# Performance work log

Hardware: AMD Instinct MI355X
Metric: run time of the kernel (lower is better)

Reference implementation:

```python
import jax, jax.numpy as jnp
import numpy as np
from jax.scipy.ndimage import map_coordinates


def _so3_exp(w):
    # Rodrigues formula, small-angle safe. w: [B,3] -> [B,3,3]
    th = jnp.linalg.norm(w, axis=-1)
    small = th < 1e-6
    ths = jnp.where(small, 1.0, th)
    A = jnp.where(small, 1.0 - th * th / 6.0, jnp.sin(ths) / ths)
    Bc = jnp.where(small, 0.5 - th * th / 24.0, (1.0 - jnp.cos(ths)) / (ths * ths))
    wx, wy, wz = w[..., 0], w[..., 1], w[..., 2]
    z = jnp.zeros_like(wx)
    K = jnp.stack([
        jnp.stack([z, -wz, wy], -1),
        jnp.stack([wz, z, -wx], -1),
        jnp.stack([-wy, wx, z], -1),
    ], -2)
    I = jnp.eye(3, dtype=w.dtype)
    return I + A[..., None, None] * K + Bc[..., None, None] * (K @ K)


def _pose(rot, xyz, rt_inv, isocenter):
    # pivot about isocenter expressed in camera frame (transform_point(rt_inv^-1, iso))
    iso_h = jnp.concatenate([isocenter, jnp.ones((1,), isocenter.dtype)])
    c = (jnp.linalg.inv(rt_inv[0]) @ iso_h)[:3]
    I4 = jnp.eye(4, dtype=rot.dtype)
    pivot = I4.at[:3, 3].set(c)
    pivot_inv = I4.at[:3, 3].set(-c)
    R = _so3_exp(rot)[0]
    t = R @ xyz[0]  # einsum('bij,bj->bi', R, xyz)
    T = I4.at[:3, :3].set(R).at[:3, 3].set(t)
    return pivot @ T @ pivot_inv


def _render(volume, k_inv, ext, sdd, height, width, n_samples):
    # DRR: cast one ray per detector pixel from the source, trilinearly sample
    # the CT volume at n_samples midpoints along source->target, accumulate.
    Rw = ext[:3, :3]
    src = ext[:3, 3]
    u = jnp.arange(width, dtype=volume.dtype) + 0.5
    v = jnp.arange(height, dtype=volume.dtype) + 0.5
    uu, vv = jnp.meshgrid(u, v, indexing='xy')  # [H,W]
    pix = jnp.stack([uu, vv, jnp.ones_like(uu)], -1)  # [H,W,3]
    dirs = jnp.einsum('ij,hwj->hwi', k_inv[0], pix)  # camera-frame ray dirs
    tgt = src + sdd[0] * jnp.einsum('ij,hwj->hwi', Rw, dirs)  # detector points in world
    seg = tgt - src  # [H,W,3]
    tvals = (jnp.arange(n_samples, dtype=volume.dtype) + 0.5) / n_samples
    pts = src + tvals[:, None, None, None] * seg[None]  # [n,H,W,3] (voxel coords)
    step = jnp.linalg.norm(seg, axis=-1) / n_samples  # [H,W] per-sample path length
    vals = map_coordinates(volume, [pts[..., 0], pts[..., 1], pts[..., 2]],
                           order=1, mode='constant', cval=0.0)  # [n,H,W]
    img = vals.sum(0) * step
    return img[None, None]  # [1,1,H,W]


def setup_inputs() -> dict:
    key = jax.random.key(0)
    k1, k2, k3 = jax.random.split(key, 3)
    D = 256
    volume = jax.random.uniform(k1, (D, D, D), dtype=jnp.float32)
    isocenter = jnp.array([128.0, 128.0, 128.0], jnp.float32)
    sdd = jnp.array([600.0], jnp.float32)
    f, cx, cy = 850.0, 256.0, 256.0
    K = jnp.array([[f, 0.0, cx], [0.0, f, cy], [0.0, 0.0, 1.0]], jnp.float32)
    k_inv = jnp.linalg.inv(K)[None]
    rt_inv = jnp.eye(4, dtype=jnp.float32).at[:3, 3].set(
        jnp.array([128.0, 128.0, -472.0], jnp.float32))[None]
    rot = 1e-8 * jax.random.normal(k2, (1, 3), jnp.float32)
    xyz = 1e-8 * jax.random.normal(k3, (1, 3), jnp.float32)
    return {"volume": volume, "isocenter": isocenter, "rt_inv": rt_inv,
            "k_inv": k_inv, "sdd": sdd, "rot": rot, "xyz": xyz,
            "height": 512, "width": 512, "n_samples": 128}


def reference(volume, isocenter, rt_inv, k_inv, sdd, rot, xyz, height, width, n_samples):
    pose = _pose(rot, xyz, rt_inv, isocenter)
    ext = rt_inv[0] @ pose  # rt_inv @ pose
    return _render(volume, k_inv, ext, sdd, height, width, n_samples)
```

## Files before the change

### kernel.cpp

```cpp
#include <hip/hip_runtime.h>
#include <hip/hip_fp16.h>
#include <math.h>

#define VD 256
#define PAIR_BYTES (VD * VD * VD * 4UL)

__device__ inline __half2 u2h2(unsigned int p) {
    return *reinterpret_cast<__half2*>(&p);
}

__device__ inline void invert4x4(const float* m, float* inv) {
    inv[0]  =  m[5]*m[10]*m[15] - m[5]*m[11]*m[14] - m[9]*m[6]*m[15] + m[9]*m[7]*m[14] + m[13]*m[6]*m[11] - m[13]*m[7]*m[10];
    inv[4]  = -m[4]*m[10]*m[15] + m[4]*m[11]*m[14] + m[8]*m[6]*m[15] - m[8]*m[7]*m[14] - m[12]*m[6]*m[11] + m[12]*m[7]*m[10];
    inv[8]  =  m[4]*m[9]*m[15]  - m[4]*m[11]*m[13] - m[8]*m[5]*m[15] + m[8]*m[7]*m[13] + m[12]*m[5]*m[11] - m[12]*m[7]*m[9];
    inv[12] = -m[4]*m[9]*m[14]  + m[4]*m[10]*m[13] + m[8]*m[5]*m[14] - m[8]*m[6]*m[13] - m[12]*m[5]*m[10] + m[12]*m[6]*m[9];
    inv[1]  = -m[1]*m[10]*m[15] + m[1]*m[11]*m[14] + m[9]*m[2]*m[15] - m[9]*m[3]*m[14] - m[13]*m[2]*m[11] + m[13]*m[3]*m[10];
    inv[5]  =  m[0]*m[10]*m[15] - m[0]*m[11]*m[14] - m[8]*m[2]*m[15] + m[8]*m[3]*m[14] + m[12]*m[2]*m[11] - m[12]*m[3]*m[10];
    inv[9]  = -m[0]*m[9]*m[15]  + m[0]*m[11]*m[13] + m[8]*m[1]*m[15] - m[8]*m[3]*m[13] - m[12]*m[1]*m[11] + m[12]*m[3]*m[9];
    inv[13] =  m[0]*m[9]*m[14]  - m[0]*m[10]*m[13] - m[8]*m[1]*m[14] + m[8]*m[2]*m[13] + m[12]*m[1]*m[10] - m[12]*m[2]*m[9];
    inv[2]  =  m[1]*m[6]*m[15]  - m[1]*m[7]*m[14]  - m[5]*m[2]*m[15] + m[5]*m[3]*m[14] + m[13]*m[2]*m[7]  - m[13]*m[3]*m[6];
    inv[6]  = -m[0]*m[6]*m[15]  + m[0]*m[7]*m[14]  + m[4]*m[2]*m[15] - m[4]*m[3]*m[14] - m[12]*m[2]*m[7]  + m[12]*m[3]*m[6];
    inv[10] =  m[0]*m[5]*m[15]  - m[0]*m[7]*m[13]  - m[4]*m[1]*m[15] + m[4]*m[3]*m[13] + m[12]*m[1]*m[7]  - m[12]*m[3]*m[5];
    inv[14] = -m[0]*m[5]*m[14]  + m[0]*m[6]*m[13]  + m[4]*m[1]*m[14] - m[4]*m[2]*m[13] - m[12]*m[1]*m[6]  + m[12]*m[2]*m[5];
    inv[3]  = -m[1]*m[6]*m[11]  + m[1]*m[7]*m[10]  + m[5]*m[2]*m[11] - m[5]*m[3]*m[10] - m[9]*m[2]*m[7]   + m[9]*m[3]*m[6];
    inv[7]  =  m[0]*m[6]*m[11]  - m[0]*m[7]*m[10]  - m[4]*m[2]*m[11] + m[4]*m[3]*m[10] + m[8]*m[2]*m[7]   - m[8]*m[3]*m[6];
    inv[11] = -m[0]*m[5]*m[11]  + m[0]*m[7]*m[9]   + m[4]*m[1]*m[11] - m[4]*m[3]*m[9]  - m[8]*m[1]*m[7]   + m[8]*m[3]*m[5];
    inv[15] =  m[0]*m[5]*m[10]  - m[0]*m[6]*m[9]   - m[4]*m[1]*m[10] + m[4]*m[2]*m[9]  + m[8]*m[1]*m[6]   - m[8]*m[2]*m[5];
    float det = m[0]*inv[0] + m[1]*inv[4] + m[2]*inv[8] + m[3]*inv[12];
    float rdet = 1.0f / det;
    for (int i = 0; i < 16; i++) inv[i] *= rdet;
}

__device__ inline void compute_pose(const float* __restrict__ iso,
                                    const float* __restrict__ rt,
                                    const float* __restrict__ kinv,
                                    const float* __restrict__ sdd,
                                    const float* __restrict__ rot,
                                    const float* __restrict__ xyz,
                                    float* M, float* src3) {
    float m[16];
    for (int i = 0; i < 16; i++) m[i] = rt[i];
    float minv[16];
    invert4x4(m, minv);
    float c0 = minv[0]*iso[0] + minv[1]*iso[1] + minv[2]*iso[2]  + minv[3];
    float c1 = minv[4]*iso[0] + minv[5]*iso[1] + minv[6]*iso[2]  + minv[7];
    float c2 = minv[8]*iso[0] + minv[9]*iso[1] + minv[10]*iso[2] + minv[11];
    float wx = rot[0], wy = rot[1], wz = rot[2];
    float th2 = wx*wx + wy*wy + wz*wz;
    float th = sqrtf(th2);
    float Ac, Bc;
    if (th < 1e-6f) { Ac = 1.0f - th2 / 6.0f; Bc = 0.5f - th2 / 24.0f; }
    else            { Ac = sinf(th) / th;     Bc = (1.0f - cosf(th)) / th2; }
    float R[9];
    R[0] = 1.0f + Bc * (-(wy*wy + wz*wz));
    R[1] = Ac * (-wz) + Bc * (wx*wy);
    R[2] = Ac * ( wy) + Bc * (wx*wz);
    R[3] = Ac * ( wz) + Bc * (wx*wy);
    R[4] = 1.0f + Bc * (-(wx*wx + wz*wz));
    R[5] = Ac * (-wx) + Bc * (wy*wz);
    R[6] = Ac * (-wy) + Bc * (wx*wz);
    R[7] = Ac * ( wx) + Bc * (wy*wz);
    R[8] = 1.0f + Bc * (-(wx*wx + wy*wy));
    float tx = R[0]*xyz[0] + R[1]*xyz[1] + R[2]*xyz[2];
    float ty = R[3]*xyz[0] + R[4]*xyz[1] + R[5]*xyz[2];
    float tz = R[6]*xyz[0] + R[7]*xyz[1] + R[8]*xyz[2];
    float pt0 = c0 + tx - (R[0]*c0 + R[1]*c1 + R[2]*c2);
    float pt1 = c1 + ty - (R[3]*c0 + R[4]*c1 + R[5]*c2);
    float pt2 = c2 + tz - (R[6]*c0 + R[7]*c1 + R[8]*c2);
    float E[12];
    for (int i = 0; i < 3; i++) {
        for (int j = 0; j < 3; j++)
            E[i*4+j] = rt[i*4+0]*R[0*3+j] + rt[i*4+1]*R[1*3+j] + rt[i*4+2]*R[2*3+j];
        E[i*4+3] = rt[i*4+0]*pt0 + rt[i*4+1]*pt1 + rt[i*4+2]*pt2 + rt[i*4+3];
    }
    float s = sdd[0];
    for (int i = 0; i < 3; i++)
        for (int j = 0; j < 3; j++)
            M[i*3+j] = s * (E[i*4+0]*kinv[0*3+j] + E[i*4+1]*kinv[1*3+j] + E[i*4+2]*kinv[2*3+j]);
    src3[0] = E[3]; src3[1] = E[7]; src3[2] = E[11];
}

__global__ __launch_bounds__(256)
void transpose_k(const float* __restrict__ in, unsigned int* __restrict__ Tp,
                 const float* __restrict__ iso, const float* __restrict__ rt,
                 const float* __restrict__ kinv, const float* __restrict__ sdd,
                 const float* __restrict__ rot, const float* __restrict__ xyz,
                 const int* __restrict__ pH, const int* __restrict__ pW) {
    __shared__ int B[6];
    __shared__ unsigned short tile[32][72];
    const int t = threadIdx.x;
    if (t == 0) {
        float M[9], src3[3];
        compute_pose(iso, rt, kinv, sdd, rot, xyz, M, src3);
        float W = (float)pW[0], H = (float)pH[0];
        float us[2] = {0.5f, W - 0.5f};
        float vs[2] = {0.5f, H - 0.5f};
        for (int a = 0; a < 3; a++) {
            float gmin = 1e30f, gmax = -1e30f;
            for (int i = 0; i < 2; i++)
                for (int j = 0; j < 2; j++) {
                    float g = M[a*3+0]*us[i] + M[a*3+1]*vs[j] + M[a*3+2];
                    gmin = fminf(gmin, g); gmax = fmaxf(gmax, g);
                }
            float sa = src3[a];
            int loi = (int)floorf(sa + fminf(0.0f, gmin)) - 4;
            int hii = (int)ceilf (sa + fmaxf(0.0f, gmax)) + 5;
            B[2*a]   = min(max(loi, 0), VD - 1);
            B[2*a+1] = min(max(hii, 0), VD - 1);
        }
    }
    __syncthreads();
    const int x0 = blockIdx.x * 64;
    const int z0 = blockIdx.y * 32;
    const int y  = blockIdx.z;
    if (x0 + 63 < B[0] || x0 > B[1] || y < B[2] || y > B[3] ||
        z0 + 31 < B[4] || z0 > B[5]) return;

    {
        const int zq = t & 7;
        const int xl = t >> 3;
        #pragma unroll
        for (int i = 0; i < 2; i++) {
            int xr = xl + 32 * i;
            const float4 f = *(const float4*)(in + (((size_t)(x0 + xr)) << 16) + (y << 8) + z0 + 4*zq);
            __half2 h01 = __float22half2_rn(make_float2(f.x, f.y));
            __half2 h23 = __float22half2_rn(make_float2(f.z, f.w));
            tile[4*zq+0][xr] = __half_as_ushort(__low2half(h01));
            tile[4*zq+1][xr] = __half_as_ushort(__high2half(h01));
            tile[4*zq+2][xr] = __half_as_ushort(__low2half(h23));
            tile[4*zq+3][xr] = __half_as_ushort(__high2half(h23));
        }
        if (t < 8) {
            int xs = min(x0 + 64, VD - 1);
            const float4 f = *(const float4*)(in + (((size_t)xs) << 16) + (y << 8) + z0 + 4*t);
            __half2 h01 = __float22half2_rn(make_float2(f.x, f.y));
            __half2 h23 = __float22half2_rn(make_float2(f.z, f.w));
            tile[4*t+0][64] = __half_as_ushort(__low2half(h01));
            tile[4*t+1][64] = __half_as_ushort(__high2half(h01));
            tile[4*t+2][64] = __half_as_ushort(__low2half(h23));
            tile[4*t+3][64] = __half_as_ushort(__high2half(h23));
        }
    }
    __syncthreads();
    {
        const int xq = t & 15;
        const int zl = t >> 4;
        #pragma unroll
        for (int i = 0; i < 2; i++) {
            int zr = zl + 16 * i;
            const uint2 aa = *reinterpret_cast<const uint2*>(&tile[zr][4*xq]);
            unsigned int h4 = tile[zr][4*xq+4];
            uint4 o;
            o.x = aa.x;
            o.y = (aa.x >> 16) | (aa.y << 16);
            o.z = aa.y;
            o.w = (aa.y >> 16) | (h4 << 16);
            *(uint4*)(Tp + (((size_t)(z0 + zr)) << 16) + (y << 8) + x0 + 4*xq) = o;
        }
    }
}

__device__ inline float sample_guarded(const unsigned int* __restrict__ Tp,
                                       float x, float y, float z) {
    float fx = floorf(x); int ix = (int)fx; float ax = x - fx;
    float fy = floorf(y); int iy = (int)fy; float ay = y - fy;
    float fz = floorf(z); int iz = (int)fz; float az = z - fz;

    float wx0v = ((unsigned)ix       < (unsigned)VD) ? (1.0f - ax) : 0.0f;
    float wx1v = ((unsigned)(ix + 1) < (unsigned)VD) ? ax : 0.0f;
    int bx = min(max(ix, 0), VD - 1);
    int sxi = ix - bx;
    float w0p = (sxi == 0) ? wx0v : ((sxi == -1) ? wx1v : 0.0f);
    float w1p = (sxi == 0) ? wx1v : 0.0f;

    float wy0 = ((unsigned)iy       < (unsigned)VD) ? (1.0f - ay) : 0.0f;
    float wy1 = ((unsigned)(iy + 1) < (unsigned)VD) ? ay : 0.0f;
    float wz0 = ((unsigned)iz       < (unsigned)VD) ? (1.0f - az) : 0.0f;
    float wz1 = ((unsigned)(iz + 1) < (unsigned)VD) ? az : 0.0f;

    int iy0 = min(max(iy, 0), VD - 1), iy1 = min(max(iy + 1, 0), VD - 1);
    int iz0 = min(max(iz, 0), VD - 1), iz1 = min(max(iz + 1, 0), VD - 1);

    int i00 = (iz0 << 16) + (iy0 << 8) + bx;
    int i01 = i00 + ((iy1 - iy0) << 8);
    int i10 = i00 + ((iz1 - iz0) << 16);
    int i11 = i10 + ((iy1 - iy0) << 8);

    __half2 h00 = u2h2(Tp[i00]);
    __half2 h01 = u2h2(Tp[i01]);
    __half2 h10 = u2h2(Tp[i10]);
    __half2 h11 = u2h2(Tp[i11]);
    float f00a = __low2float(h00), f00b = __high2float(h00);
    float f01a = __low2float(h01), f01b = __high2float(h01);
    float f10a = __low2float(h10), f10b = __high2float(h10);
    float f11a = __low2float(h11), f11b = __high2float(h11);

    float cx00 = fmaf(f00a, w0p, f00b * w1p);
    float cx01 = fmaf(f01a, w0p, f01b * w1p);
    float cx10 = fmaf(f10a, w0p, f10b * w1p);
    float cx11 = fmaf(f11a, w0p, f11b * w1p);

    float cy0 = fmaf(cx00, wy0, cx01 * wy1);
    float cy1 = fmaf(cx10, wy0, cx11 * wy1);
    return cy0 * wz0 + cy1 * wz1;
}

__global__ __launch_bounds__(256)
void render_pair(const unsigned int* __restrict__ Tp,
                 const float* __restrict__ iso, const float* __restrict__ rt,
                 const float* __restrict__ kinv, const float* __restrict__ sdd,
                 const float* __restrict__ rot, const float* __restrict__ xyz,
                 const int* __restrict__ pW, const int* __restrict__ pN,
                 float* __restrict__ out, int total) {
    __shared__ float S[12];
    if (threadIdx.x == 0) {
        float M[9], src3[3];
        compute_pose(iso, rt, kinv, sdd, rot, xyz, M, src3);
        for (int i = 0; i < 9; i++) S[i] = M[i];
        S[9] = src3[0]; S[10] = src3[1]; S[11] = src3[2];
    }
    __syncthreads();
    int tid = blockIdx.x * 256 + threadIdx.x;
    if (tid >= total) return;
    const int W = pW[0];
    const int N = pN[0];
    int w = tid % W;
    int h = tid / W;
    float u = (float)w + 0.5f;
    float v = (float)h + 0.5f;

    float gx = S[0]*u + S[1]*v + S[2];
    float gy = S[3]*u + S[4]*v + S[5];
    float gz = S[6]*u + S[7]*v + S[8];
    float sx = S[9], sy = S[10], sz = S[11];
    float len = sqrtf(gx*gx + gy*gy + gz*gz);
    float invN = 1.0f / (float)N;

    float t0 = 0.0f, t1 = 1.0f;
    float tA = 0.0f, tB = 1.0f;
    {
        const float HI = (float)(VD - 1) - 0.01f;
        float s3[3] = {sx, sy, sz};
        float g3[3] = {gx, gy, gz};
        for (int a = 0; a < 3; a++) {
            float g = g3[a], s = s3[a];
            if (fabsf(g) > 1e-20f) {
                float rg = 1.0f / g;
                float ta = (-1.0f - s) * rg;
                float tb = ((float)VD - s) * rg;
                t0 = fmaxf(t0, fminf(ta, tb));
                t1 = fminf(t1, fmaxf(ta, tb));
                float tc = (0.0f - s) * rg;
                float td = (HI - s) * rg;
                tA = fmaxf(tA, fminf(tc, td));
                tB = fminf(tB, fmaxf(tc, td));
            } else {
                if (s <= -1.0f || s >= (float)VD) t1 = -1.0f;
                if (s < 0.0f || s > HI)           tB = -2.0f;
            }
        }
    }
    int k0 = (int)floorf(t0 * (float)N - 0.5f) - 1;
    int k1 = (int)ceilf (t1 * (float)N - 0.5f) + 1;
    if (k0 < 0) k0 = 0;
    if (k1 > N - 1) k1 = N - 1;
    int kA = (int)ceilf (tA * (float)N - 0.5f) + 1;
    int kB = (int)floorf(tB * (float)N - 0.5f) - 1;
    kA = max(kA, k0);
    kB = min(kB, k1);

    float acc = 0.0f;
    int headEnd = min(kA - 1, k1);
    for (int k = k0; k <= headEnd; k++) {
        float t = ((float)k + 0.5f) * invN;
        acc += sample_guarded(Tp, fmaf(t, gx, sx), fmaf(t, gy, sy), fmaf(t, gz, sz));
    }
    if (kA <= kB) {
        float dx = gx * invN, dy = gy * invN, dz = gz * invN;
        float tS = ((float)kA + 0.5f) * invN;
        float x = fmaf(tS, gx, sx);
        float y = fmaf(tS, gy, sy);
        float z = fmaf(tS, gz, sz);
        #pragma unroll 2
        for (int k = kA; k <= kB; k++) {
            int ix = (int)x; float ax = x - (float)ix;
            int iy = (int)y; float ay = y - (float)iy;
            int iz = (int)z; float az = z - (float)iz;
            int idx = (iz << 16) + (iy << 8) + ix;
            unsigned int p00 = Tp[idx];
            unsigned int p01 = Tp[idx + 256];
            unsigned int p10 = Tp[idx + 65536];
            unsigned int p11 = Tp[idx + 65536 + 256];
            __half2 h00 = u2h2(p00);
            __half2 h01 = u2h2(p01);
            __half2 h10 = u2h2(p10);
            __half2 h11 = u2h2(p11);
            __half2 ay2 = __float2half2_rn(ay);
            __half2 az2 = __float2half2_rn(az);
            __half2 cy0 = __hfma2(__hsub2(h01, h00), ay2, h00);
            __half2 cy1 = __hfma2(__hsub2(h11, h10), ay2, h10);
            __half2 cz  = __hfma2(__hsub2(cy1, cy0), az2, cy0);
            float a = __low2float(cz), b = __high2float(cz);
            acc += fmaf(b - a, ax, a);
            x += dx; y += dy; z += dz;
        }
    }
    int tailStart = max(kB + 1, kA);
    for (int k = tailStart; k <= k1; k++) {
        float t = ((float)k + 0.5f) * invN;
        acc += sample_guarded(Tp, fmaf(t, gx, sx), fmaf(t, gy, sy), fmaf(t, gz, sz));
    }
    out[tid] = acc * len * invN;
}

__global__ __launch_bounds__(256)
void render_direct(const float* __restrict__ vol,
                   const float* __restrict__ iso, const float* __restrict__ rt,
                   const float* __restrict__ kinv, const float* __restrict__ sdd,
                   const float* __restrict__ rot, const float* __restrict__ xyz,
                   const int* __restrict__ pW, const int* __restrict__ pN,
                   float* __restrict__ out, int total) {
    __shared__ float S[12];
    if (threadIdx.x == 0) {
        float M[9], src3[3];
        compute_pose(iso, rt, kinv, sdd, rot, xyz, M, src3);
        for (int i = 0; i < 9; i++) S[i] = M[i];
        S[9] = src3[0]; S[10] = src3[1]; S[11] = src3[2];
    }
    __syncthreads();
    int tid = blockIdx.x * 256 + threadIdx.x;
    if (tid >= total) return;
    const int W = pW[0];
    const int N = pN[0];
    int w = tid % W;
    int h = tid / W;
    float u = (float)w + 0.5f;
    float v = (float)h + 0.5f;
    float gx = S[0]*u + S[1]*v + S[2];
    float gy = S[3]*u + S[4]*v + S[5];
    float gz = S[6]*u + S[7]*v + S[8];
    float sx = S[9], sy = S[10], sz = S[11];
    float len = sqrtf(gx*gx + gy*gy + gz*gz);
    float invN = 1.0f / (float)N;
    float acc = 0.0f;
    for (int k = 0; k < N; k++) {
        float t = ((float)k + 0.5f) * invN;
        float x = fmaf(t, gx, sx);
        float y = fmaf(t, gy, sy);
        float z = fmaf(t, gz, sz);
        float fx = floorf(x); int ix = (int)fx; float ax = x - fx;
        float fy = floorf(y); int iy = (int)fy; float ay = y - fy;
        float fz = floorf(z); int iz = (int)fz; float az = z - fz;
        float wx0 = ((unsigned)ix       < (unsigned)VD) ? (1.0f - ax) : 0.0f;
        float wx1 = ((unsigned)(ix + 1) < (unsigned)VD) ? ax : 0.0f;
        float wy0 = ((unsigned)iy       < (unsigned)VD) ? (1.0f - ay) : 0.0f;
        float wy1 = ((unsigned)(iy + 1) < (unsigned)VD) ? ay : 0.0f;
        float wz0 = ((unsigned)iz       < (unsigned)VD) ? (1.0f - az) : 0.0f;
        float wz1 = ((unsigned)(iz + 1) < (unsigned)VD) ? az : 0.0f;
        int ix0 = min(max(ix, 0), VD - 1), ix1 = min(max(ix + 1, 0), VD - 1);
        int iy0 = min(max(iy, 0), VD - 1), iy1 = min(max(iy + 1, 0), VD - 1);
        int iz0 = min(max(iz, 0), VD - 1), iz1 = min(max(iz + 1, 0), VD - 1);
        int X0 = ix0 << 16, X1 = ix1 << 16;
        int Y0 = iy0 << 8,  Y1 = iy1 << 8;
        float v000 = vol[X0 + Y0 + iz0];
        float v001 = vol[X0 + Y0 + iz1];
        float v010 = vol[X0 + Y1 + iz0];
        float v011 = vol[X0 + Y1 + iz1];
        float v100 = vol[X1 + Y0 + iz0];
        float v101 = vol[X1 + Y0 + iz1];
        float v110 = vol[X1 + Y1 + iz0];
        float v111 = vol[X1 + Y1 + iz1];
        float c00 = fmaf(v000, wz0, v001 * wz1);
        float c01 = fmaf(v010, wz0, v011 * wz1);
        float c10 = fmaf(v100, wz0, v101 * wz1);
        float c11 = fmaf(v110, wz0, v111 * wz1);
        float c0  = fmaf(c00, wy0, c01 * wy1);
        float c1  = fmaf(c10, wy0, c11 * wy1);
        acc += fmaf(c0, wx0, c1 * wx1);
    }
    out[tid] = acc * len * invN;
}

extern "C" void kernel_launch(void* const* d_in, const int* in_sizes, int n_in,
                              void* d_out, int out_size, void* d_ws, size_t ws_size,
                              hipStream_t stream) {
    const float* vol  = (const float*)d_in[0];
    const float* iso  = (const float*)d_in[1];
    const float* rt   = (const float*)d_in[2];
    const float* kinv = (const float*)d_in[3];
    const float* sdd  = (const float*)d_in[4];
    const float* rot  = (const float*)d_in[5];
    const float* xyz  = (const float*)d_in[6];
    const int* pH = (const int*)d_in[7];
    const int* pW = (const int*)d_in[8];
    const int* pN = (const int*)d_in[9];
    float* out = (float*)d_out;
    int total = out_size;

    if (ws_size >= PAIR_BYTES) {
        unsigned int* Tp = (unsigned int*)d_ws;
        transpose_k<<<dim3(4, 8, 256), 256, 0, stream>>>(vol, Tp, iso, rt, kinv, sdd, rot, xyz, pH, pW);
        render_pair<<<(total + 255) / 256, 256, 0, stream>>>(Tp, iso, rt, kinv, sdd, rot, xyz, pW, pN, out, total);
    } else {
        render_direct<<<(total + 255) / 256, 256, 0, stream>>>(vol, iso, rt, kinv, sdd, rot, xyz, pW, pN, out, total);
    }
}
```

Measured before the change: 146.1 us.

## Fuse transpose and render into one cooperative kernel with grid sync

Merges the half-precision transpose pass and the ray-marching render into a single persistent cooperative kernel of 512 blocks, using a grid-wide barrier between the two phases. This removes one kernel launch and the gap between the two launches. The interior sampling loop also changes from packed half2 interpolation to fp32 interpolation after converting the halves. The trade-offs are grid-sync overhead, a fixed grid size that may limit render parallelism, and more fp32 ALU work per sample. The direct fp32 fallback path is removed, so the code now assumes the workspace is large enough.

Result: slower. 229.7 us (+57.3%).

```diff
diff --git a/kernel.cpp b/kernel.cpp
--- a/kernel.cpp
+++ b/kernel.cpp
@@ -1,9 +1,13 @@
 #include <hip/hip_runtime.h>
 #include <hip/hip_fp16.h>
+#include <hip/hip_cooperative_groups.h>
 #include <math.h>
+
+namespace cg = cooperative_groups;
 
 #define VD 256
 #define PAIR_BYTES (VD * VD * VD * 4UL)
+#define NBLK 512
 
 __device__ inline __half2 u2h2(unsigned int p) {
     return *reinterpret_cast<__half2*>(&p);
@@ -80,6 +84,240 @@
     src3[0] = E[3]; src3[1] = E[7]; src3[2] = E[11];
 }
 
+__device__ inline float sample_guarded(const unsigned int* __restrict__ Tp,
+                                       float x, float y, float z) {
+    float fx = floorf(x); int ix = (int)fx; float ax = x - fx;
+    float fy = floorf(y); int iy = (int)fy; float ay = y - fy;
+    float fz = floorf(z); int iz = (int)fz; float az = z - fz;
+
+    float wx0v = ((unsigned)ix       < (unsigned)VD) ? (1.0f - ax) : 0.0f;
+    float wx1v = ((unsigned)(ix + 1) < (unsigned)VD) ? ax : 0.0f;
+    int bx = min(max(ix, 0), VD - 1);
+    int sxi = ix - bx;
+    float w0p = (sxi == 0) ? wx0v : ((sxi == -1) ? wx1v : 0.0f);
+    float w1p = (sxi == 0) ? wx1v : 0.0f;
+
+    float wy0 = ((unsigned)iy       < (unsigned)VD) ? (1.0f - ay) : 0.0f;
+    float wy1 = ((unsigned)(iy + 1) < (unsigned)VD) ? ay : 0.0f;
+    float wz0 = ((unsigned)iz       < (unsigned)VD) ? (1.0f - az) : 0.0f;
+    float wz1 = ((unsigned)(iz + 1) < (unsigned)VD) ? az : 0.0f;
+
+    int iy0 = min(max(iy, 0), VD - 1), iy1 = min(max(iy + 1, 0), VD - 1);
+    int iz0 = min(max(iz, 0), VD - 1), iz1 = min(max(iz + 1, 0), VD - 1);
+
+    int i00 = (iz0 << 16) + (iy0 << 8) + bx;
+    int i01 = i00 + ((iy1 - iy0) << 8);
+    int i10 = i00 + ((iz1 - iz0) << 16);
+    int i11 = i10 + ((iy1 - iy0) << 8);
+
+    __half2 h00 = u2h2(Tp[i00]);
+    __half2 h01 = u2h2(Tp[i01]);
+    __half2 h10 = u2h2(Tp[i10]);
+    __half2 h11 = u2h2(Tp[i11]);
+    float f00a = __low2float(h00), f00b = __high2float(h00);
+    float f01a = __low2float(h01), f01b = __high2float(h01);
+    float f10a = __low2float(h10), f10b = __high2float(h10);
+    float f11a = __low2float(h11), f11b = __high2float(h11);
+
+    float cx00 = fmaf(f00a, w0p, f00b * w1p);
+    float cx01 = fmaf(f01a, w0p, f01b * w1p);
+    float cx10 = fmaf(f10a, w0p, f10b * w1p);
+    float cx11 = fmaf(f11a, w0p, f11b * w1p);
+
+    float cy0 = fmaf(cx00, wy0, cx01 * wy1);
+    float cy1 = fmaf(cx10, wy0, cx11 * wy1);
+    return cy0 * wz0 + cy1 * wz1;
+}
+
+__device__ inline float render_pixel(const unsigned int* __restrict__ Tp,
+                                     const float* S, int pix, int W, int N) {
+    int w = pix % W;
+    int h = pix / W;
+    float u = (float)w + 0.5f;
+    float v = (float)h + 0.5f;
+    float gx = S[0]*u + S[1]*v + S[2];
+    float gy = S[3]*u + S[4]*v + S[5];
+    float gz = S[6]*u + S[7]*v + S[8];
+    float sx = S[9], sy = S[10], sz = S[11];
+    float len = sqrtf(gx*gx + gy*gy + gz*gz);
+    float invN = 1.0f / (float)N;
+
+    float t0 = 0.0f, t1 = 1.0f;
+    float tA = 0.0f, tB = 1.0f;
+    {
+        const float HI = (float)(VD - 1) - 0.01f;
+        float s3[3] = {sx, sy, sz};
+        float g3[3] = {gx, gy, gz};
+        for (int a = 0; a < 3; a++) {
+            float g = g3[a], s = s3[a];
+            if (fabsf(g) > 1e-20f) {
+                float rg = 1.0f / g;
+                float ta = (-1.0f - s) * rg;
+                float tb = ((float)VD - s) * rg;
+                t0 = fmaxf(t0, fminf(ta, tb));
+                t1 = fminf(t1, fmaxf(ta, tb));
+                float tc = (0.0f - s) * rg;
+                float td = (HI - s) * rg;
+                tA = fmaxf(tA, fminf(tc, td));
+                tB = fminf(tB, fmaxf(tc, td));
+            } else {
+                if (s <= -1.0f || s >= (float)VD) t1 = -1.0f;
+                if (s < 0.0f || s > HI)           tB = -2.0f;
+            }
+        }
+    }
+    int k0 = (int)floorf(t0 * (float)N - 0.5f) - 1;
+    int k1 = (int)ceilf (t1 * (float)N - 0.5f) + 1;
+    if (k0 < 0) k0 = 0;
+    if (k1 > N - 1) k1 = N - 1;
+    int kA = (int)ceilf (tA * (float)N - 0.5f) + 1;
+    int kB = (int)floorf(tB * (float)N - 0.5f) - 1;
+    kA = max(kA, k0);
+    kB = min(kB, k1);
+
+    float acc = 0.0f;
+    int headEnd = min(kA - 1, k1);
+    for (int k = k0; k <= headEnd; k++) {
+        float t = ((float)k + 0.5f) * invN;
+        acc += sample_guarded(Tp, fmaf(t, gx, sx), fmaf(t, gy, sy), fmaf(t, gz, sz));
+    }
+    if (kA <= kB) {
+        float dx = gx * invN, dy = gy * invN, dz = gz * invN;
+        float tS = ((float)kA + 0.5f) * invN;
+        float x = fmaf(tS, gx, sx);
+        float y = fmaf(tS, gy, sy);
+        float z = fmaf(tS, gz, sz);
+        #pragma unroll 2
+        for (int k = kA; k <= kB; k++) {
+            int ix = (int)x; float ax = x - (float)ix;
+            int iy = (int)y; float ay = y - (float)iy;
+            int iz = (int)z; float az = z - (float)iz;
+            int idx = (iz << 16) + (iy << 8) + ix;
+            unsigned int p00 = Tp[idx];
+            unsigned int p01 = Tp[idx + 256];
+            unsigned int p10 = Tp[idx + 65536];
+            unsigned int p11 = Tp[idx + 65536 + 256];
+            __half2 h00 = u2h2(p00);
+            __half2 h01 = u2h2(p01);
+            __half2 h10 = u2h2(p10);
+            __half2 h11 = u2h2(p11);
+            float f00a = __low2float(h00), f00b = __high2float(h00);
+            float f01a = __low2float(h01), f01b = __high2float(h01);
+            float f10a = __low2float(h10), f10b = __high2float(h10);
+            float f11a = __low2float(h11), f11b = __high2float(h11);
+            float cx00 = fmaf(f00b - f00a, ax, f00a);
+            float cx01 = fmaf(f01b - f01a, ax, f01a);
+            float cx10 = fmaf(f10b - f10a, ax, f10a);
+            float cx11 = fmaf(f11b - f11a, ax, f11a);
+            float cy0 = fmaf(cx01 - cx00, ay, cx00);
+            float cy1 = fmaf(cx11 - cx10, ay, cx10);
+            acc += fmaf(cy1 - cy0, az, cy0);
+            x += dx; y += dy; z += dz;
+        }
+    }
+    int tailStart = max(kB + 1, kA);
+    for (int k = tailStart; k <= k1; k++) {
+        float t = ((float)k + 0.5f) * invN;
+        acc += sample_guarded(Tp, fmaf(t, gx, sx), fmaf(t, gy, sy), fmaf(t, gz, sz));
+    }
+    return acc * len * invN;
+}
+
+__global__ __launch_bounds__(256, 4)
+void fused_k(const float* __restrict__ in, unsigned int* __restrict__ Tp,
+             const float* __restrict__ iso, const float* __restrict__ rt,
+             const float* __restrict__ kinv, const float* __restrict__ sdd,
+             const float* __restrict__ rot, const float* __restrict__ xyz,
+             const int* __restrict__ pH, const int* __restrict__ pW,
+             const int* __restrict__ pN, float* __restrict__ out, int total) {
+    __shared__ float S[12];
+    __shared__ int B[6];
+    __shared__ unsigned short tile[32][72];
+    const int t = threadIdx.x;
+    if (t == 0) {
+        float M[9], src3[3];
+        compute_pose(iso, rt, kinv, sdd, rot, xyz, M, src3);
+        for (int i = 0; i < 9; i++) S[i] = M[i];
+        S[9] = src3[0]; S[10] = src3[1]; S[11] = src3[2];
+        float W = (float)pW[0], H = (float)pH[0];
+        float us[2] = {0.5f, W - 0.5f};
+        float vs[2] = {0.5f, H - 0.5f};
+        for (int a = 0; a < 3; a++) {
+            float gmin = 1e30f, gmax = -1e30f;
+            for (int i = 0; i < 2; i++)
+                for (int j = 0; j < 2; j++) {
+                    float g = M[a*3+0]*us[i] + M[a*3+1]*vs[j] + M[a*3+2];
+                    gmin = fminf(gmin, g); gmax = fmaxf(gmax, g);
+                }
+            float sa = src3[a];
+            int loi = (int)floorf(sa + fminf(0.0f, gmin)) - 4;
+            int hii = (int)ceilf (sa + fmaxf(0.0f, gmax)) + 5;
+            B[2*a]   = min(max(loi, 0), VD - 1);
+            B[2*a+1] = min(max(hii, 0), VD - 1);
+        }
+    }
+    __syncthreads();
+
+    const int nb = gridDim.x;
+    for (int tid8 = blockIdx.x; tid8 < 8192; tid8 += nb) {
+        const int x0 = (tid8 & 3) * 64;
+        const int z0 = ((tid8 >> 2) & 7) * 32;
+        const int y  = tid8 >> 5;
+        bool active = !(x0 + 63 < B[0] || x0 > B[1] || y < B[2] || y > B[3] ||
+                        z0 + 31 < B[4] || z0 > B[5]);
+        if (active) {
+            const int zq = t & 7;
+            const int xl = t >> 3;
+            #pragma unroll
+            for (int i = 0; i < 2; i++) {
+                int xr = xl + 32 * i;
+                const float4 f = *(const float4*)(in + (((size_t)(x0 + xr)) << 16) + (y << 8) + z0 + 4*zq);
+                __half2 h01 = __float22half2_rn(make_float2(f.x, f.y));
+                __half2 h23 = __float22half2_rn(make_float2(f.z, f.w));
+                tile[4*zq+0][xr] = __half_as_ushort(__low2half(h01));
+                tile[4*zq+1][xr] = __half_as_ushort(__high2half(h01));
+                tile[4*zq+2][xr] = __half_as_ushort(__low2half(h23));
+                tile[4*zq+3][xr] = __half_as_ushort(__high2half(h23));
+            }
+            if (t < 8) {
+                int xs = min(x0 + 64, VD - 1);
+                const float4 f = *(const float4*)(in + (((size_t)xs) << 16) + (y << 8) + z0 + 4*t);
+                __half2 h01 = __float22half2_rn(make_float2(f.x, f.y));
+                __half2 h23 = __float22half2_rn(make_float2(f.z, f.w));
+                tile[4*t+0][64] = __half_as_ushort(__low2half(h01));
+                tile[4*t+1][64] = __half_as_ushort(__high2half(h01));
+                tile[4*t+2][64] = __half_as_ushort(__low2half(h23));
+                tile[4*t+3][64] = __half_as_ushort(__high2half(h23));
+            }
+        }
+        __syncthreads();
+        if (active) {
+            const int xq = t & 15;
+            const int zl = t >> 4;
+            #pragma unroll
+            for (int i = 0; i < 2; i++) {
+                int zr = zl + 16 * i;
+                const uint2 aa = *reinterpret_cast<const uint2*>(&tile[zr][4*xq]);
+                unsigned int h4 = tile[zr][4*xq+4];
+                uint4 o;
+                o.x = aa.x;
+                o.y = (aa.x >> 16) | (aa.y << 16);
+                o.z = aa.y;
+                o.w = (aa.y >> 16) | (h4 << 16);
+                *(uint4*)(Tp + (((size_t)(z0 + zr)) << 16) + (y << 8) + x0 + 4*xq) = o;
+            }
+        }
+        __syncthreads();
+    }
+
+    cg::this_grid().sync();
+
+    const int W = pW[0];
+    const int N = pN[0];
+    for (int pix = blockIdx.x * 256 + t; pix < total; pix += nb * 256)
+        out[pix] = render_pixel(Tp, S, pix, W, N);
+}
+
 __global__ __launch_bounds__(256)
 void transpose_k(const float* __restrict__ in, unsigned int* __restrict__ Tp,
                  const float* __restrict__ iso, const float* __restrict__ rt,
@@ -115,7 +353,6 @@
     const int y  = blockIdx.z;
     if (x0 + 63 < B[0] || x0 > B[1] || y < B[2] || y > B[3] ||
         z0 + 31 < B[4] || z0 > B[5]) return;
-
     {
         const int zq = t & 7;
         const int xl = t >> 3;
@@ -160,51 +397,6 @@
     }
 }
 
-__device__ inline float sample_guarded(const unsigned int* __restrict__ Tp,
-                                       float x, float y, float z) {
-    float fx = floorf(x); int ix = (int)fx; float ax = x - fx;
-    float fy = floorf(y); int iy = (int)fy; float ay = y - fy;
-    float fz = floorf(z); int iz = (int)fz; float az = z - fz;
-
-    float wx0v = ((unsigned)ix       < (unsigned)VD) ? (1.0f - ax) : 0.0f;
-    float wx1v = ((unsigned)(ix + 1) < (unsigned)VD) ? ax : 0.0f;
-    int bx = min(max(ix, 0), VD - 1);
-    int sxi = ix - bx;
-    float w0p = (sxi == 0) ? wx0v : ((sxi == -1) ? wx1v : 0.0f);
-    float w1p = (sxi == 0) ? wx1v : 0.0f;
-
-    float wy0 = ((unsigned)iy       < (unsigned)VD) ? (1.0f - ay) : 0.0f;
-    float wy1 = ((unsigned)(iy + 1) < (unsigned)VD) ? ay : 0.0f;
-    float wz0 = ((unsigned)iz       < (unsigned)VD) ? (1.0f - az) : 0.0f;
-    float wz1 = ((unsigned)(iz + 1) < (unsigned)VD) ? az : 0.0f;
-
-    int iy0 = min(max(iy, 0), VD - 1), iy1 = min(max(iy + 1, 0), VD - 1);
-    int iz0 = min(max(iz, 0), VD - 1), iz1 = min(max(iz + 1, 0), VD - 1);
-
-    int i00 = (iz0 << 16) + (iy0 << 8) + bx;
-    int i01 = i00 + ((iy1 - iy0) << 8);
-    int i10 = i00 + ((iz1 - iz0) << 16);
-    int i11 = i10 + ((iy1 - iy0) << 8);
-
-    __half2 h00 = u2h2(Tp[i00]);
-    __half2 h01 = u2h2(Tp[i01]);
-    __half2 h10 = u2h2(Tp[i10]);
-    __half2 h11 = u2h2(Tp[i11]);
-    float f00a = __low2float(h00), f00b = __high2float(h00);
-    float f01a = __low2float(h01), f01b = __high2float(h01);
-    float f10a = __low2float(h10), f10b = __high2float(h10);
-    float f11a = __low2float(h11), f11b = __high2float(h11);
-
-    float cx00 = fmaf(f00a, w0p, f00b * w1p);
-    float cx01 = fmaf(f01a, w0p, f01b * w1p);
-    float cx10 = fmaf(f10a, w0p, f10b * w1p);
-    float cx11 = fmaf(f11a, w0p, f11b * w1p);
-
-    float cy0 = fmaf(cx00, wy0, cx01 * wy1);
-    float cy1 = fmaf(cx10, wy0, cx11 * wy1);
-    return cy0 * wz0 + cy1 * wz1;
-}
-
 __global__ __launch_bounds__(256)
 void render_pair(const unsigned int* __restrict__ Tp,
                  const float* __restrict__ iso, const float* __restrict__ rt,
@@ -222,163 +414,7 @@
     __syncthreads();
     int tid = blockIdx.x * 256 + threadIdx.x;
     if (tid >= total) return;
-    const int W = pW[0];
-    const int N = pN[0];
-    int w = tid % W;
-    int h = tid / W;
-    float u = (float)w + 0.5f;
-    float v = (float)h + 0.5f;
-
-    float gx = S[0]*u + S[1]*v + S[2];
-    float gy = S[3]*u + S[4]*v + S[5];
-    float gz = S[6]*u + S[7]*v + S[8];
-    float sx = S[9], sy = S[10], sz = S[11];
-    float len = sqrtf(gx*gx + gy*gy + gz*gz);
-    float invN = 1.0f / (float)N;
-
-    float t0 = 0.0f, t1 = 1.0f;
-    float tA = 0.0f, tB = 1.0f;
-    {
-        const float HI = (float)(VD - 1) - 0.01f;
-        float s3[3] = {sx, sy, sz};
-        float g3[3] = {gx, gy, gz};
-        for (int a = 0; a < 3; a++) {
-            float g = g3[a], s = s3[a];
-            if (fabsf(g) > 1e-20f) {
-                float rg = 1.0f / g;
-                float ta = (-1.0f - s) * rg;
-                float tb = ((float)VD - s) * rg;
-                t0 = fmaxf(t0, fminf(ta, tb));
-                t1 = fminf(t1, fmaxf(ta, tb));
-                float tc = (0.0f - s) * rg;
-                float td = (HI - s) * rg;
-                tA = fmaxf(tA, fminf(tc, td));
-                tB = fminf(tB, fmaxf(tc, td));
-            } else {
-                if (s <= -1.0f || s >= (float)VD) t1 = -1.0f;
-                if (s < 0.0f || s > HI)           tB = -2.0f;
-            }
-        }
-    }
-    int k0 = (int)floorf(t0 * (float)N - 0.5f) - 1;
-    int k1 = (int)ceilf (t1 * (float)N - 0.5f) + 1;
-    if (k0 < 0) k0 = 0;
-    if (k1 > N - 1) k1 = N - 1;
-    int kA = (int)ceilf (tA * (float)N - 0.5f) + 1;
-    int kB = (int)floorf(tB * (float)N - 0.5f) - 1;
-    kA = max(kA, k0);
-    kB = min(kB, k1);
-
-    float acc = 0.0f;
-    int headEnd = min(kA - 1, k1);
-    for (int k = k0; k <= headEnd; k++) {
-        float t = ((float)k + 0.5f) * invN;
-        acc += sample_guarded(Tp, fmaf(t, gx, sx), fmaf(t, gy, sy), fmaf(t, gz, sz));
-    }
-    if (kA <= kB) {
-        float dx = gx * invN, dy = gy * invN, dz = gz * invN;
-        float tS = ((float)kA + 0.5f) * invN;
-        float x = fmaf(tS, gx, sx);
-        float y = fmaf(tS, gy, sy);
-        float z = fmaf(tS, gz, sz);
-        #pragma unroll 2
-        for (int k = kA; k <= kB; k++) {
-            int ix = (int)x; float ax = x - (float)ix;
-            int iy = (int)y; float ay = y - (float)iy;
-            int iz = (int)z; float az = z - (float)iz;
-            int idx = (iz << 16) + (iy << 8) + ix;
-            unsigned int p00 = Tp[idx];
-            unsigned int p01 = Tp[idx + 256];
-            unsigned int p10 = Tp[idx + 65536];
-            unsigned int p11 = Tp[idx + 65536 + 256];
-            __half2 h00 = u2h2(p00);
-            __half2 h01 = u2h2(p01);
-            __half2 h10 = u2h2(p10);
-            __half2 h11 = u2h2(p11);
-            __half2 ay2 = __float2half2_rn(ay);
-            __half2 az2 = __float2half2_rn(az);
-            __half2 cy0 = __hfma2(__hsub2(h01, h00), ay2, h00);
-            __half2 cy1 = __hfma2(__hsub2(h11, h10), ay2, h10);
-            __half2 cz  = __hfma2(__hsub2(cy1, cy0), az2, cy0);
-            float a = __low2float(cz), b = __high2float(cz);
-            acc += fmaf(b - a, ax, a);
-            x += dx; y += dy; z += dz;
-        }
-    }
-    int tailStart = max(kB + 1, kA);
-    for (int k = tailStart; k <= k1; k++) {
-        float t = ((float)k + 0.5f) * invN;
-        acc += sample_guarded(Tp, fmaf(t, gx, sx), fmaf(t, gy, sy), fmaf(t, gz, sz));
-    }
-    out[tid] = acc * len * invN;
-}
-
-__global__ __launch_bounds__(256)
-void render_direct(const float* __restrict__ vol,
-                   const float* __restrict__ iso, const float* __restrict__ rt,
-                   const float* __restrict__ kinv, const float* __restrict__ sdd,
-                   const float* __restrict__ rot, const float* __restrict__ xyz,
-                   const int* __restrict__ pW, const int* __restrict__ pN,
-                   float* __restrict__ out, int total) {
-    __shared__ float S[12];
-    if (threadIdx.x == 0) {
-        float M[9], src3[3];
-        compute_pose(iso, rt, kinv, sdd, rot, xyz, M, src3);
-        for (int i = 0; i < 9; i++) S[i] = M[i];
-        S[9] = src3[0]; S[10] = src3[1]; S[11] = src3[2];
-    }
-    __syncthreads();
-    int tid = blockIdx.x * 256 + threadIdx.x;
-    if (tid >= total) return;
-    const int W = pW[0];
-    const int N = pN[0];
-    int w = tid % W;
-    int h = tid / W;
-    float u = (float)w + 0.5f;
-    float v = (float)h + 0.5f;
-    float gx = S[0]*u + S[1]*v + S[2];
-    float gy = S[3]*u + S[4]*v + S[5];
-    float gz = S[6]*u + S[7]*v + S[8];
-    float sx = S[9], sy = S[10], sz = S[11];
-    float len = sqrtf(gx*gx + gy*gy + gz*gz);
-    float invN = 1.0f / (float)N;
-    float acc = 0.0f;
-    for (int k = 0; k < N; k++) {
-        float t = ((float)k + 0.5f) * invN;
-        float x = fmaf(t, gx, sx);
-        float y = fmaf(t, gy, sy);
-        float z = fmaf(t, gz, sz);
-        float fx = floorf(x); int ix = (int)fx; float ax = x - fx;
-        float fy = floorf(y); int iy = (int)fy; float ay = y - fy;
-        float fz = floorf(z); int iz = (int)fz; float az = z - fz;
-        float wx0 = ((unsigned)ix       < (unsigned)VD) ? (1.0f - ax) : 0.0f;
-        float wx1 = ((unsigned)(ix + 1) < (unsigned)VD) ? ax : 0.0f;
-        float wy0 = ((unsigned)iy       < (unsigned)VD) ? (1.0f - ay) : 0.0f;
-        float wy1 = ((unsigned)(iy + 1) < (unsigned)VD) ? ay : 0.0f;
-        float wz0 = ((unsigned)iz       < (unsigned)VD) ? (1.0f - az) : 0.0f;
-        float wz1 = ((unsigned)(iz + 1) < (unsigned)VD) ? az : 0.0f;
-        int ix0 = min(max(ix, 0), VD - 1), ix1 = min(max(ix + 1, 0), VD - 1);
-        int iy0 = min(max(iy, 0), VD - 1), iy1 = min(max(iy + 1, 0), VD - 1);
-        int iz0 = min(max(iz, 0), VD - 1), iz1 = min(max(iz + 1, 0), VD - 1);
-        int X0 = ix0 << 16, X1 = ix1 << 16;
-        int Y0 = iy0 << 8,  Y1 = iy1 << 8;
-        float v000 = vol[X0 + Y0 + iz0];
-        float v001 = vol[X0 + Y0 + iz1];
-        float v010 = vol[X0 + Y1 + iz0];
-        float v011 = vol[X0 + Y1 + iz1];
-        float v100 = vol[X1 + Y0 + iz0];
-        float v101 = vol[X1 + Y0 + iz1];
-        float v110 = vol[X1 + Y1 + iz0];
-        float v111 = vol[X1 + Y1 + iz1];
-        float c00 = fmaf(v000, wz0, v001 * wz1);
-        float c01 = fmaf(v010, wz0, v011 * wz1);
-        float c10 = fmaf(v100, wz0, v101 * wz1);
-        float c11 = fmaf(v110, wz0, v111 * wz1);
-        float c0  = fmaf(c00, wy0, c01 * wy1);
-        float c1  = fmaf(c10, wy0, c11 * wy1);
-        acc += fmaf(c0, wx0, c1 * wx1);
-    }
-    out[tid] = acc * len * invN;
+    out[tid] = render_pixel(Tp, S, tid, pW[0], pN[0]);
 }
 
 extern "C" void kernel_launch(void* const* d_in, const int* in_sizes, int n_in,
@@ -396,12 +432,17 @@
     const int* pN = (const int*)d_in[9];
     float* out = (float*)d_out;
     int total = out_size;
-
-    if (ws_size >= PAIR_BYTES) {
-        unsigned int* Tp = (unsigned int*)d_ws;
+    unsigned int* Tp = (unsigned int*)d_ws;
+
+    void* args[] = { (void*)&vol, (void*)&Tp, (void*)&iso, (void*)&rt,
+                     (void*)&kinv, (void*)&sdd, (void*)&rot, (void*)&xyz,
+                     (void*)&pH, (void*)&pW, (void*)&pN, (void*)&out,
+                     (void*)&total };
+    hipError_t err = hipLaunchCooperativeKernel((const void*)fused_k,
+                                                dim3(NBLK), dim3(256),
+                                                args, 0, stream);
+    if (err != hipSuccess) {
         transpose_k<<<dim3(4, 8, 256), 256, 0, stream>>>(vol, Tp, iso, rt, kinv, sdd, rot, xyz, pH, pW);
         render_pair<<<(total + 255) / 256, 256, 0, stream>>>(Tp, iso, rt, kinv, sdd, rot, xyz, pW, pN, out, total);
-    } else {
-        render_direct<<<(total + 255) / 256, 256, 0, stream>>>(vol, iso, rt, kinv, sdd, rot, xyz, pW, pN, out, total);
-    }
-}
+    }
+}
```
